# Kernel tuning notes

Measured on AMD Instinct MI355X. Metric: run time of the kernel, lower is better.

## Reference

```python
import jax, jax.numpy as jnp
import numpy as np
from jax import lax

D = 384      # embd_d
L = 4        # num_blocks
B = 64
SHW, THW = 24, 12
NS, NT = SHW * SHW, THW * THW   # 576, 144
EPS = 1e-5


def _ln(x, g, b):
    mu = jnp.mean(x, axis=-1, keepdims=True)
    var = jnp.mean(jnp.square(x - mu), axis=-1, keepdims=True)
    return (x - mu) * lax.rsqrt(var + EPS) * g + b


def setup_inputs() -> dict:
    key = jax.random.key(0)
    ks = iter(jax.random.split(key, 64))
    f32 = jnp.float32
    def nrm(shape, s=0.02):
        return jax.random.normal(next(ks), shape, dtype=f32) * s
    inp = {
        'search': jax.random.normal(next(ks), (B, NS, D), dtype=f32),
        'target': jax.random.normal(next(ks), (B, NT, D), dtype=f32),
        # learned tokens / positional params
        'cls': nrm((1, 1, D), 1.0),
        'search_pos': nrm((1, NS, D), 0.5),
        'target_pos': nrm((1, NT, D), 0.5),
        # stacked per-block params [L, ...]
        'ln1_g': jnp.ones((L, D), f32), 'ln1_b': jnp.zeros((L, D), f32),
        'Wq': nrm((L, D, D)), 'bq': jnp.zeros((L, D), f32),
        'Wk': nrm((L, D, D)), 'bk': jnp.zeros((L, D), f32),
        'Wv': nrm((L, D, D)), 'bv': jnp.zeros((L, D), f32),
        'ln2_g': jnp.ones((L, D), f32), 'ln2_b': jnp.zeros((L, D), f32),
        'W1': nrm((L, D, 2 * D)), 'b1': jnp.zeros((L, 2 * D), f32),
        'W2': nrm((L, 2 * D, D)), 'b2': jnp.zeros((L, D), f32),
        # head
        'lnf_g': jnp.ones((D,), f32), 'lnf_b': jnp.zeros((D,), f32),
        'Wl1': nrm((D, D)), 'bl1': jnp.zeros((D,), f32),
        'Wl2': nrm((D, 1)), 'bl2': jnp.zeros((1,), f32),
    }
    return inp


def reference(search, target, cls, search_pos, target_pos,
              ln1_g, ln1_b, Wq, bq, Wk, bk, Wv, bv,
              ln2_g, ln2_b, W1, b1, W2, b2,
              lnf_g, lnf_b, Wl1, bl1, Wl2, bl2):
    scale = D ** (-0.5)  # note: full embed dim, as in source
    x = jnp.concatenate([
        jnp.broadcast_to(cls, (B, 1, D)),
        search + search_pos,
        target + target_pos,
    ], axis=1)  # [B, 1+Ns+Nt, D]

    def block(x, p):
        l1g, l1b, wq, bq_, wk, bk_, wv, bv_, l2g, l2b, w1, b1_, w2, b2_ = p
        y = _ln(x, l1g, l1b)
        q = y @ wq + bq_
        k = y @ wk + bk_
        v = y @ wv + bv_
        attn = jax.nn.softmax(jnp.einsum('bid,bjd->bij', q, k) * scale, axis=-1)
        x = x + jnp.einsum('bij,bjd->bid', attn, v)
        h = _ln(x, l2g, l2b)
        x = x + (jax.nn.gelu(h @ w1 + b1_, approximate=False) @ w2 + b2_)
        return x, None

    x, _ = lax.scan(block, x, (ln1_g, ln1_b, Wq, bq, Wk, bk, Wv, bv,
                               ln2_g, ln2_b, W1, b1, W2, b2))
    h = _ln(x[:, 0], lnf_g, lnf_b)          # cls token [B, D]
    h = jax.nn.relu(h @ Wl1 + bl1)
    return h @ Wl2 + bl2                     # [B, 1]
```

## Files before the change

### kernel.cpp

```cpp
#include <hip/hip_runtime.h>
#include <hip/hip_bf16.h>
#include <math.h>

#define DD 384
#define NBATCH 64
#define NSEQ 721
#define NROWS (NBATCH*NSEQ)
#define NLAYER 4
#define VTW 736

typedef __bf16 bf16_t;
typedef __bf16 bf16x8 __attribute__((ext_vector_type(8)));
typedef float  f32x4  __attribute__((ext_vector_type(4)));

static __device__ __forceinline__ void split_bf16(float v, bf16_t& h, bf16_t& l) {
    h = (bf16_t)v;
    l = (bf16_t)(v - (float)h);
}
static __device__ __forceinline__ bf16x8 bzero8() {
    bf16x8 v = {(bf16_t)0.f,(bf16_t)0.f,(bf16_t)0.f,(bf16_t)0.f,
                (bf16_t)0.f,(bf16_t)0.f,(bf16_t)0.f,(bf16_t)0.f};
    return v;
}
static __device__ __forceinline__ void gload16(const void* g, void* l) {
    __builtin_amdgcn_global_load_lds(
        (const __attribute__((address_space(1))) unsigned int*)g,
        (__attribute__((address_space(3))) unsigned int*)l, 16, 0, 0);
}
static __device__ __forceinline__ int xcd_swz(int nwg) {
    int orig = blockIdx.x;
    int q = nwg >> 3, r = nwg & 7;
    int xcd = orig & 7, within = orig >> 3;
    int base = (xcd < r) ? xcd*(q+1) : r*(q+1) + (xcd - r)*q;
    return base + within;
}
static __device__ __forceinline__ void ln_from_partials(const float* ss, const float* ss2,
                                                        int row, float& mu, float& rstd) {
    float s = 0.f, q2 = 0.f;
    #pragma unroll
    for (int k = 0; k < 6; ++k) { s += ss[k*NROWS + row]; q2 += ss2[k*NROWS + row]; }
    mu = s * (1.f/DD);
    float var = q2 * (1.f/DD) - mu*mu;
    rstd = rsqrtf(var + 1e-5f);
}

__global__ __launch_bounds__(256) void build_x_kernel(const float* __restrict__ search,
                               const float* __restrict__ target,
                               const float* __restrict__ cls,
                               const float* __restrict__ spos,
                               const float* __restrict__ tpos,
                               bf16_t* __restrict__ xh, bf16_t* __restrict__ xl,
                               float* __restrict__ wss, float* __restrict__ wss2) {
    int wave = threadIdx.x >> 6, lane = threadIdx.x & 63;
    int row = blockIdx.x * 4 + wave;
    if (row >= NROWS) return;
    int b = row / NSEQ, n = row % NSEQ;
    float s = 0.f, q2 = 0.f;
    #pragma unroll
    for (int i = 0; i < 6; ++i) {
        int d = lane + 64*i;
        float val;
        if (n == 0)        val = cls[d];
        else if (n <= 576) val = search[((size_t)b*576 + (n-1))*DD + d] + spos[(size_t)(n-1)*DD + d];
        else               val = target[((size_t)b*144 + (n-577))*DD + d] + tpos[(size_t)(n-577)*DD + d];
        bf16_t h, l;
        split_bf16(val, h, l);
        xh[(size_t)row*DD + d] = h;
        xl[(size_t)row*DD + d] = l;
        s += val; q2 += val*val;
    }
    #pragma unroll
    for (int m = 1; m < 64; m <<= 1) { s += __shfl_xor(s, m); q2 += __shfl_xor(q2, m); }
    if (lane == 0) {
        wss[row] = s; wss2[row] = q2;
        #pragma unroll
        for (int k = 1; k < 6; ++k) { wss[k*NROWS + row] = 0.f; wss2[k*NROWS + row] = 0.f; }
    }
}

__global__ void transpose_split_kernel(const float* __restrict__ src,
                                       const float* __restrict__ g,
                                       bf16_t* __restrict__ dh,
                                       bf16_t* __restrict__ dl,
                                       int K, int N) {
    int idx = blockIdx.x * blockDim.x + threadIdx.x;
    if (idx >= K*N) return;
    int k = idx / N, n = idx % N;
    float v = src[idx];
    if (g) v *= g[k];
    bf16_t h, l;
    split_bf16(v, h, l);
    dh[(size_t)n*K + k] = h;
    dl[(size_t)n*K + k] = l;
}

__global__ void colsum_kernel(const float* __restrict__ W, const float* __restrict__ g,
                              const float* __restrict__ b, const float* __restrict__ bias,
                              float* __restrict__ c1, float* __restrict__ c2,
                              int K, int N, int outStride, int outOff) {
    int l = blockIdx.y;
    int n = blockIdx.x * 256 + threadIdx.x;
    if (n >= N) return;
    const float* Wl = W + (size_t)l*K*N;
    const float* gl = g + (size_t)l*K;
    const float* bl = b + (size_t)l*K;
    float s1 = 0.f, s2 = 0.f;
    for (int k = 0; k < K; ++k) {
        float w = Wl[(size_t)k*N + n];
        s1 = fmaf(gl[k], w, s1);
        s2 = fmaf(bl[k], w, s2);
    }
    c1[(size_t)l*outStride + outOff + n] = s1;
    c2[(size_t)l*outStride + outOff + n] = s2 + bias[(size_t)l*N + n];
}

static __device__ __forceinline__ void gemm_core(
        const bf16_t* __restrict__ ah, const bf16_t* __restrict__ al,
        const bf16_t* __restrict__ bh, const bf16_t* __restrict__ bl,
        bf16_t (&ls)[2][32][64][8],
        int m0, int n0, int K, f32x4 (&acc)[4][4]) {
    int t = threadIdx.x;
    int w = t >> 6, lane = t & 63;
    int c = lane & 15, g = lane >> 4;
    int wr = w >> 1, wc = w & 1;
    const bf16_t* src0 = (w==0) ? ah : (w==1) ? al : (w==2) ? bh : bl;
    int base_rc = (w < 2) ? m0 : n0;
    const bf16_t* srcbase = src0 + (size_t)(base_rc + c)*K + 8*g;

    int ksteps = K >> 5;
    #pragma unroll
    for (int i = 0; i < 8; ++i)
        gload16(srcbase + (size_t)(16*i)*K, &ls[0][w*8 + i][0][0]);

    for (int kt = 0; kt < ksteps; ++kt) {
        int cur = kt & 1;
        if (kt + 1 < ksteps) {
            int k0n = (kt + 1) << 5;
            #pragma unroll
            for (int i = 0; i < 8; ++i)
                gload16(srcbase + (size_t)(16*i)*K + k0n, &ls[cur^1][w*8 + i][0][0]);
            asm volatile("s_waitcnt vmcnt(8)" ::: "memory");
        } else {
            asm volatile("s_waitcnt vmcnt(0)" ::: "memory");
        }
        __builtin_amdgcn_sched_barrier(0);
        __builtin_amdgcn_s_barrier();
        __builtin_amdgcn_sched_barrier(0);
        bf16x8 af_h[4], af_l[4], bf_h[4], bf_l[4];
        #pragma unroll
        for (int i = 0; i < 4; ++i) {
            af_h[i] = *(const bf16x8*)&ls[cur][     4*wr + i][lane][0];
            af_l[i] = *(const bf16x8*)&ls[cur][ 8 + 4*wr + i][lane][0];
            bf_h[i] = *(const bf16x8*)&ls[cur][16 + 4*wc + i][lane][0];
            bf_l[i] = *(const bf16x8*)&ls[cur][24 + 4*wc + i][lane][0];
        }
        #pragma unroll
        for (int i = 0; i < 4; ++i)
            #pragma unroll
            for (int j = 0; j < 4; ++j) {
                acc[i][j] = __builtin_amdgcn_mfma_f32_16x16x32_bf16(af_h[i], bf_h[j], acc[i][j], 0,0,0);
                acc[i][j] = __builtin_amdgcn_mfma_f32_16x16x32_bf16(af_h[i], bf_l[j], acc[i][j], 0,0,0);
                acc[i][j] = __builtin_amdgcn_mfma_f32_16x16x32_bf16(af_l[i], bf_h[j], acc[i][j], 0,0,0);
            }
        __builtin_amdgcn_sched_barrier(0);
        __builtin_amdgcn_s_barrier();
    }
}

__global__ __launch_bounds__(256, 2) void gemm_qkv(
        const bf16_t* __restrict__ ah, const bf16_t* __restrict__ al,
        const bf16_t* __restrict__ bh, const bf16_t* __restrict__ bl,
        const float* __restrict__ ss, const float* __restrict__ ss2,
        const float* __restrict__ c1, const float* __restrict__ c2,
        bf16_t* __restrict__ qout, bf16_t* __restrict__ kout,
        bf16_t* __restrict__ vth, bf16_t* __restrict__ vtl,
        int M, int nwg) {
    __shared__ __align__(16) bf16_t ls[2][32][64][8];
    int wgid = xcd_swz(nwg);
    int m0 = (wgid / 9) * 128, n0 = (wgid % 9) * 128;
    f32x4 zero4 = {0.f,0.f,0.f,0.f};
    f32x4 acc[4][4];
    #pragma unroll
    for (int i = 0; i < 4; ++i)
        #pragma unroll
        for (int j = 0; j < 4; ++j) acc[i][j] = zero4;
    gemm_core(ah, al, bh, bl, ls, m0, n0, DD, acc);

    int t = threadIdx.x, w = t >> 6, lane = t & 63;
    int c = lane & 15, g = lane >> 4;
    int wr = w >> 1, wc = w & 1;
    float rmu[16], rrs[16];
    #pragma unroll
    for (int i = 0; i < 4; ++i)
        #pragma unroll
        for (int r = 0; r < 4; ++r) {
            int row = m0 + 64*wr + 16*i + 4*g + r;
            float mu = 0.f, rstd = 1.f;
            if (row < M) ln_from_partials(ss, ss2, row, mu, rstd);
            rmu[i*4+r] = mu; rrs[i*4+r] = rstd;
        }
    int seg = n0 / 384;
    int segoff = seg * 384;
    #pragma unroll
    for (int j = 0; j < 4; ++j) {
        int nglob = n0 + 64*wc + 16*j + c;
        int nloc = nglob - segoff;
        float C1 = c1[nglob], C2 = c2[nglob];
        #pragma unroll
        for (int i = 0; i < 4; ++i) {
            int rbase = m0 + 64*wr + 16*i + 4*g;
            #pragma unroll
            for (int r = 0; r < 4; ++r) {
                int row = rbase + r;
                if (row >= M) continue;
                float val = rrs[i*4+r]*(acc[i][j][r] - rmu[i*4+r]*C1) + C2;
                if (seg == 0) {
                    qout[(size_t)row*DD + nloc] = (bf16_t)val;
                } else if (seg == 1) {
                    kout[(size_t)row*DD + nloc] = (bf16_t)val;
                } else {
                    int bl_ = row / NSEQ;
                    int tok = row - bl_*NSEQ;
                    bf16_t h, l;
                    split_bf16(val, h, l);
                    size_t o = ((size_t)(bl_*DD + nloc))*VTW + tok;
                    vth[o] = h;
                    vtl[o] = l;
                }
            }
        }
    }
}

template<int EPI, int NT>
__global__ __launch_bounds__(256, 2) void gemm_mfma(
        const bf16_t* __restrict__ ah, const bf16_t* __restrict__ al,
        const bf16_t* __restrict__ bh, const bf16_t* __restrict__ bl,
        const float* __restrict__ ss, const float* __restrict__ ss2,
        const float* __restrict__ c1, const float* __restrict__ c2,
        const float* __restrict__ bias,
        const bf16_t* __restrict__ resh, const bf16_t* __restrict__ resl,
        bf16_t* __restrict__ o1, bf16_t* __restrict__ o2,
        float* __restrict__ wss, float* __restrict__ wss2,
        int M, int N, int K, int nwg) {
    __shared__ __align__(16) bf16_t ls[2][32][64][8];
    int wgid = xcd_swz(nwg);
    int m0 = (wgid / NT) * 128, n0 = (wgid % NT) * 128;
    f32x4 zero4 = {0.f,0.f,0.f,0.f};
    f32x4 acc[4][4];
    #pragma unroll
    for (int i = 0; i < 4; ++i)
        #pragma unroll
        for (int j = 0; j < 4; ++j) acc[i][j] = zero4;
    gemm_core(ah, al, bh, bl, ls, m0, n0, K, acc);

    int t = threadIdx.x, w = t >> 6, lane = t & 63;
    int c = lane & 15, g = lane >> 4;
    int wr = w >> 1, wc = w & 1;

    if (EPI == 2) {
        float rmu[16], rrs[16];
        #pragma unroll
        for (int i = 0; i < 4; ++i)
            #pragma unroll
            for (int r = 0; r < 4; ++r) {
                int row = m0 + 64*wr + 16*i + 4*g + r;
                float mu = 0.f, rstd = 1.f;
                if (row < M) ln_from_partials(ss, ss2, row, mu, rstd);
                rmu[i*4+r] = mu; rrs[i*4+r] = rstd;
            }
        #pragma unroll
        for (int j = 0; j < 4; ++j) {
            int n = n0 + 64*wc + 16*j + c;
            float C1 = c1[n], C2 = c2[n];
            #pragma unroll
            for (int i = 0; i < 4; ++i) {
                int rbase = m0 + 64*wr + 16*i + 4*g;
                #pragma unroll
                for (int r = 0; r < 4; ++r) {
                    int row = rbase + r;
                    if (row >= M) continue;
                    float val = rrs[i*4+r]*(acc[i][j][r] - rmu[i*4+r]*C1) + C2;
                    val = 0.5f*val*(1.0f + erff(val*0.70710678118654752f));
                    bf16_t h, l;
                    split_bf16(val, h, l);
                    size_t o = (size_t)row*N + n;
                    o1[o] = h;
                    o2[o] = l;
                }
            }
        }
    } else {
        int slot = (wgid % NT) + 3*wc;
        #pragma unroll
        for (int i = 0; i < 4; ++i)
            #pragma unroll
            for (int r = 0; r < 4; ++r) {
                int row = m0 + 64*wr + 16*i + 4*g + r;
                if (row >= M) continue;
                float s = 0.f, q2 = 0.f;
                #pragma unroll
                for (int j = 0; j < 4; ++j) {
                    int n = n0 + 64*wc + 16*j + c;
                    size_t o = (size_t)row*N + n;
                    float val = acc[i][j][r] + bias[n] + (float)resh[o] + (float)resl[o];
                    bf16_t h, l;
                    split_bf16(val, h, l);
                    o1[o] = h;
                    o2[o] = l;
                    s += val; q2 += val*val;
                }
                #pragma unroll
                for (int m = 1; m < 16; m <<= 1) { s += __shfl_xor(s, m); q2 += __shfl_xor(q2, m); }
                if (c == 0) {
                    wss[slot*NROWS + row] = s;
                    wss2[slot*NROWS + row] = q2;
                }
            }
    }
}

__global__ __launch_bounds__(256, 2) void attn_mfma(
        const bf16_t* __restrict__ qh, const bf16_t* __restrict__ kh,
        const bf16_t* __restrict__ vth, const bf16_t* __restrict__ vtl,
        bf16_t* __restrict__ xh, bf16_t* __restrict__ xl,
        float* __restrict__ wss, float* __restrict__ wss2, int nwg) {
    __shared__ __align__(16) char smem[73728];
    bf16_t* kf = (bf16_t*)smem;
    char* vhp = smem + 24576;
    char* vlp = smem + 49152;

    int t = threadIdx.x, w = t >> 6, lane = t & 63;
    int c = lane & 15, g = lane >> 4;
    int wgid = xcd_swz(nwg);
    int bl_ = wgid / 12;
    int q0 = (wgid % 12) * 64;
    size_t bb = (size_t)bl_ * NSEQ;
    int qrow = q0 + 16*w + c;
    bool qok = (qrow < NSEQ);
    const float scale = 0.05103103630798287f;
    int vswz = (c ^ (c >> 2)) & 3;
    int dma_dd  = lane >> 2;
    int dma_kv8 = (lane & 3) ^ ((dma_dd ^ (dma_dd >> 2)) & 3);

    bf16x8 qf[12];
    #pragma unroll
    for (int ks = 0; ks < 12; ++ks) {
        if (qok) qf[ks] = *(const bf16x8*)(qh + (bb + qrow)*DD + 32*ks + 8*g);
        else     qf[ks] = bzero8();
    }

    f32x4 zero4 = {0.f,0.f,0.f,0.f};
    f32x4 oacc[24];
    #pragma unroll
    for (int i = 0; i < 24; ++i) oacc[i] = zero4;
    float m_run = -1e30f, l_run = 0.f;

    #pragma unroll
    for (int i = 0; i < 6; ++i) {
        int s = i*4 + w;
        int ks = s >> 1, mf = s & 1;
        gload16(kh + (bb + (size_t)(16*mf + c))*DD + 32*ks + 8*g, kf + s*512);
    }

    for (int kt = 0; kt < 23; ++kt) {
        int kv0 = kt * 32;
        asm volatile("s_waitcnt vmcnt(0)" ::: "memory");
        __builtin_amdgcn_s_barrier();
        #pragma unroll
        for (int i = 0; i < 6; ++i) {
            int s = i*4 + w;
            size_t gro = ((size_t)(bl_*DD + 16*s + dma_dd))*VTW + kv0 + 8*dma_kv8;
            gload16(vth + gro, (bf16_t*)vhp + s*512);
            gload16(vtl + gro, (bf16_t*)vlp + s*512);
        }
        f32x4 sacc[2];
        sacc[0] = zero4; sacc[1] = zero4;
        #pragma unroll
        for (int ks = 0; ks < 12; ++ks) {
            bf16x8 a0 = *(const bf16x8*)(kf + ((size_t)(2*ks+0)*64 + lane)*8);
            bf16x8 a1 = *(const bf16x8*)(kf + ((size_t)(2*ks+1)*64 + lane)*8);
            sacc[0] = __builtin_amdgcn_mfma_f32_16x16x32_bf16(a0, qf[ks], sacc[0], 0,0,0);
            sacc[1] = __builtin_amdgcn_mfma_f32_16x16x32_bf16(a1, qf[ks], sacc[1], 0,0,0);
        }
        float p[2][4];
        float mx = -1e30f;
        #pragma unroll
        for (int mf = 0; mf < 2; ++mf)
            #pragma unroll
            for (int r = 0; r < 4; ++r) {
                float sv = sacc[mf][r] * scale;
                int kv = kv0 + 16*mf + 4*g + r;
                if (kv >= NSEQ) sv = -1e30f;
                p[mf][r] = sv;
                mx = fmaxf(mx, sv);
            }
        mx = fmaxf(mx, __shfl_xor(mx, 16));
        mx = fmaxf(mx, __shfl_xor(mx, 32));
        float m_new = fmaxf(m_run, mx);
        float corr = __expf(m_run - m_new);
        float psum = 0.f;
        #pragma unroll
        for (int mf = 0; mf < 2; ++mf)
            #pragma unroll
            for (int r = 0; r < 4; ++r) {
                float pv = __expf(p[mf][r] - m_new);
                p[mf][r] = pv;
                psum += pv;
            }
        psum += __shfl_xor(psum, 16);
        psum += __shfl_xor(psum, 32);
        l_run = l_run * corr + psum;
        m_run = m_new;
        #pragma unroll
        for (int i = 0; i < 24; ++i) oacc[i] *= corr;
        bf16x8 ph, pl;
        #pragma unroll
        for (int mf = 0; mf < 2; ++mf)
            #pragma unroll
            for (int r = 0; r < 4; ++r) {
                bf16_t hh, ll;
                split_bf16(p[mf][r], hh, ll);
                ph[mf*4 + r] = hh;
                pl[mf*4 + r] = ll;
            }
        asm volatile("s_waitcnt vmcnt(0)" ::: "memory");
        __builtin_amdgcn_s_barrier();
        if (kt + 1 < 23) {
            int kv0n = kv0 + 32;
            #pragma unroll
            for (int i = 0; i < 6; ++i) {
                int s = i*4 + w;
                int ks = s >> 1, mf = s & 1;
                gload16(kh + (bb + (size_t)(kv0n + 16*mf + c))*DD + 32*ks + 8*g, kf + s*512);
            }
        }
        #pragma unroll
        for (int mf = 0; mf < 24; ++mf) {
            int dr = 16*mf + c;
            const char* vb  = vhp + dr*64;
            const char* vb2 = vlp + dr*64;
            int o0 = ((((g>>1)     ^ vswz) << 4) | (8*(g&1)));
            int o1 = (((2 + (g>>1)) ^ vswz) << 4) | (8*(g&1));
            union { uint2 u[2]; bf16x8 v; } va, vc2;
            va.u[0]  = *(const uint2*)(vb  + o0);
            va.u[1]  = *(const uint2*)(vb  + o1);
            vc2.u[0] = *(const uint2*)(vb2 + o0);
            vc2.u[1] = *(const uint2*)(vb2 + o1);
            oacc[mf] = __builtin_amdgcn_mfma_f32_16x16x32_bf16(va.v,  ph, oacc[mf], 0,0,0);
            oacc[mf] = __builtin_amdgcn_mfma_f32_16x16x32_bf16(va.v,  pl, oacc[mf], 0,0,0);
            oacc[mf] = __builtin_amdgcn_mfma_f32_16x16x32_bf16(vc2.v, ph, oacc[mf], 0,0,0);
        }
    }
    float inv = 1.f / l_run;
    float s = 0.f, q2 = 0.f;
    if (qok) {
        bf16_t* xhr = xh + (bb + qrow)*DD;
        bf16_t* xlr = xl + (bb + qrow)*DD;
        #pragma unroll
        for (int mf = 0; mf < 24; ++mf)
            #pragma unroll
            for (int r = 0; r < 4; ++r) {
                int d = 16*mf + 4*g + r;
                float xv = (float)xhr[d] + (float)xlr[d] + oacc[mf][r]*inv;
                bf16_t h, l;
                split_bf16(xv, h, l);
                xhr[d] = h;
                xlr[d] = l;
                s += xv; q2 += xv*xv;
            }
    }
    s += __shfl_xor(s, 16);  q2 += __shfl_xor(q2, 16);
    s += __shfl_xor(s, 32);  q2 += __shfl_xor(q2, 32);
    if (qok && g == 0) {
        int rowL = bl_*NSEQ + qrow;
        wss[rowL] = s; wss2[rowL] = q2;
        #pragma unroll
        for (int k = 1; k < 6; ++k) { wss[k*NROWS + rowL] = 0.f; wss2[k*NROWS + rowL] = 0.f; }
    }
}

__global__ __launch_bounds__(384) void head_kernel(const bf16_t* __restrict__ xh,
    const bf16_t* __restrict__ xl,
    const float* __restrict__ g, const float* __restrict__ bb,
    const float* __restrict__ Wl1, const float* __restrict__ bl1,
    const float* __restrict__ Wl2, const float* __restrict__ bl2,
    float* __restrict__ outp) {
    __shared__ float yv[384];
    __shared__ float r1[6], r2[6], r3[6];
    int b = blockIdx.x, t = threadIdx.x;
    size_t o = (size_t)b*NSEQ*DD + t;
    float v = (float)xh[o] + (float)xl[o];
    float s = v;
    #pragma unroll
    for (int m = 1; m < 64; m <<= 1) s += __shfl_xor(s, m);
    if ((t & 63) == 0) r1[t>>6] = s;
    __syncthreads();
    float mu = (r1[0]+r1[1]+r1[2]+r1[3]+r1[4]+r1[5]) * (1.f/384.f);
    float dd = v - mu;
    float sq = dd*dd;
    #pragma unroll
    for (int m = 1; m < 64; m <<= 1) sq += __shfl_xor(sq, m);
    if ((t & 63) == 0) r2[t>>6] = sq;
    __syncthreads();
    float var = (r2[0]+r2[1]+r2[2]+r2[3]+r2[4]+r2[5]) * (1.f/384.f);
    float rstd = rsqrtf(var + 1e-5f);
    yv[t] = dd*rstd*g[t] + bb[t];
    __syncthreads();
    float acc = bl1[t];
    for (int d2 = 0; d2 < 384; d2++) acc = fmaf(yv[d2], Wl1[d2*384 + t], acc);
    acc = fmaxf(acc, 0.f);
    float oo = acc * Wl2[t];
    #pragma unroll
    for (int m = 1; m < 64; m <<= 1) oo += __shfl_xor(oo, m);
    if ((t & 63) == 0) r3[t>>6] = oo;
    __syncthreads();
    if (t == 0) outp[b] = r3[0]+r3[1]+r3[2]+r3[3]+r3[4]+r3[5] + bl2[0];
}

extern "C" void kernel_launch(void* const* d_in, const int* in_sizes, int n_in,
                              void* d_out, int out_size, void* d_ws, size_t ws_size,
                              hipStream_t stream) {
    const float* search = (const float*)d_in[0];
    const float* target = (const float*)d_in[1];
    const float* cls    = (const float*)d_in[2];
    const float* spos   = (const float*)d_in[3];
    const float* tpos   = (const float*)d_in[4];
    const float* ln1_g  = (const float*)d_in[5];
    const float* ln1_b  = (const float*)d_in[6];
    const float* Wq     = (const float*)d_in[7];
    const float* bq     = (const float*)d_in[8];
    const float* Wk     = (const float*)d_in[9];
    const float* bk     = (const float*)d_in[10];
    const float* Wv     = (const float*)d_in[11];
    const float* bv     = (const float*)d_in[12];
    const float* ln2_g  = (const float*)d_in[13];
    const float* ln2_b  = (const float*)d_in[14];
    const float* W1     = (const float*)d_in[15];
    const float* b1     = (const float*)d_in[16];
    const float* W2     = (const float*)d_in[17];
    const float* b2     = (const float*)d_in[18];
    const float* lnf_g  = (const float*)d_in[19];
    const float* lnf_b  = (const float*)d_in[20];
    const float* Wl1    = (const float*)d_in[21];
    const float* bl1    = (const float*)d_in[22];
    const float* Wl2    = (const float*)d_in[23];
    const float* bl2    = (const float*)d_in[24];

    size_t off = 0;
    char* base = (char*)d_ws;
    auto alloc = [&](size_t bytes) -> void* {
        void* p = base + off;
        off += (bytes + 255) & ~(size_t)255;
        return p;
    };

    bf16_t* xh = (bf16_t*)alloc((size_t)NROWS * DD * 2);
    bf16_t* xl = (bf16_t*)alloc((size_t)NROWS * DD * 2);
    float* ssum  = (float*)alloc((size_t)6*NROWS*4);
    float* ssum2 = (float*)alloc((size_t)6*NROWS*4);

    const int SQKV = 1152*DD;
    const int SM = DD*768;
    bf16_t* wqkvh = (bf16_t*)alloc((size_t)4*SQKV*2);
    bf16_t* wqkvl = (bf16_t*)alloc((size_t)4*SQKV*2);
    bf16_t* w1h = (bf16_t*)alloc((size_t)4*SM*2);
    bf16_t* w1l = (bf16_t*)alloc((size_t)4*SM*2);
    bf16_t* w2h = (bf16_t*)alloc((size_t)4*SM*2);
    bf16_t* w2l = (bf16_t*)alloc((size_t)4*SM*2);
    float* cqkv1 = (float*)alloc((size_t)4*1152*4);
    float* cqkv2 = (float*)alloc((size_t)4*1152*4);
    float* cm11  = (float*)alloc((size_t)4*768*4);
    float* cm12  = (float*)alloc((size_t)4*768*4);

    const size_t qB  = (size_t)NSEQ*DD*2;
    const size_t vB  = (size_t)DD*VTW*2;
    const size_t mB  = (size_t)NSEQ*768*2;
    const size_t perB = 2*qB + 2*vB;
    size_t avail = (ws_size > off + 262144) ? (ws_size - off - 262144) : 0;
    int G = (int)(avail / perB);
    if (G > NBATCH) G = NBATCH;
    if (G < 1) G = 1;

    char* U = (char*)alloc(perB * G);
    bf16_t* qhB  = (bf16_t*)U;
    bf16_t* khB  = (bf16_t*)(U + qB*G);
    bf16_t* vth  = (bf16_t*)(U + 2*qB*G);
    bf16_t* vtl  = (bf16_t*)(U + 2*qB*G + vB*G);
    bf16_t* midh = (bf16_t*)U;
    bf16_t* midl = (bf16_t*)(U + mB*G);

    build_x_kernel<<<(NROWS+3)/4, 256, 0, stream>>>(search, target, cls, spos, tpos,
                                                    xh, xl, ssum, ssum2);

    const int SQ = DD*DD;
    for (int l = 0; l < NLAYER; ++l) {
        bf16_t* dsth = wqkvh + (size_t)l*SQKV;
        bf16_t* dstl = wqkvl + (size_t)l*SQKV;
        transpose_split_kernel<<<(SQ+255)/256, 256, 0, stream>>>(Wq + (size_t)l*SQ, ln1_g + l*DD, dsth,          dstl,          DD, DD);
        transpose_split_kernel<<<(SQ+255)/256, 256, 0, stream>>>(Wk + (size_t)l*SQ, ln1_g + l*DD, dsth + 384*DD, dstl + 384*DD, DD, DD);
        transpose_split_kernel<<<(SQ+255)/256, 256, 0, stream>>>(Wv + (size_t)l*SQ, ln1_g + l*DD, dsth + 768*DD, dstl + 768*DD, DD, DD);
        transpose_split_kernel<<<(SM+255)/256, 256, 0, stream>>>(W1 + (size_t)l*SM, ln2_g + l*DD, w1h + (size_t)l*SM, w1l + (size_t)l*SM, DD, 768);
        transpose_split_kernel<<<(SM+255)/256, 256, 0, stream>>>(W2 + (size_t)l*SM, nullptr,      w2h + (size_t)l*SM, w2l + (size_t)l*SM, 768, DD);
    }
    colsum_kernel<<<dim3(2, NLAYER), 256, 0, stream>>>(Wq, ln1_g, ln1_b, bq, cqkv1, cqkv2, DD, DD, 1152, 0);
    colsum_kernel<<<dim3(2, NLAYER), 256, 0, stream>>>(Wk, ln1_g, ln1_b, bk, cqkv1, cqkv2, DD, DD, 1152, 384);
    colsum_kernel<<<dim3(2, NLAYER), 256, 0, stream>>>(Wv, ln1_g, ln1_b, bv, cqkv1, cqkv2, DD, DD, 1152, 768);
    colsum_kernel<<<dim3(3, NLAYER), 256, 0, stream>>>(W1, ln2_g, ln2_b, b1, cm11, cm12, DD, 768, 768, 0);

    for (int l = 0; l < NLAYER; ++l) {
        for (int b0 = 0; b0 < NBATCH; b0 += G) {
            int cb = (NBATCH - b0 < G) ? (NBATCH - b0) : G;
            int Mc = cb * NSEQ;
            bf16_t* xch = xh + (size_t)b0 * NSEQ * DD;
            bf16_t* xcl = xl + (size_t)b0 * NSEQ * DD;
            float* ssc  = ssum  + (size_t)b0 * NSEQ;
            float* ssc2 = ssum2 + (size_t)b0 * NSEQ;
            int mtiles = (Mc + 127)/128;
            int nwgQKV = 9*mtiles, nwgM1 = 6*mtiles, nwgM2 = 3*mtiles, nwgA = 12*cb;

            gemm_qkv<<<nwgQKV, 256, 0, stream>>>(xch, xcl,
                    wqkvh + (size_t)l*SQKV, wqkvl + (size_t)l*SQKV,
                    ssc, ssc2, cqkv1 + l*1152, cqkv2 + l*1152,
                    qhB, khB, vth, vtl, Mc, nwgQKV);
            attn_mfma<<<nwgA, 256, 0, stream>>>(qhB, khB, vth, vtl, xch, xcl,
                    ssc, ssc2, nwgA);
            gemm_mfma<2,6><<<nwgM1, 256, 0, stream>>>(xch, xcl,
                    w1h + (size_t)l*SM, w1l + (size_t)l*SM,
                    ssc, ssc2, cm11 + l*768, cm12 + l*768, nullptr,
                    nullptr, nullptr, midh, midl, nullptr, nullptr, Mc, 768, DD, nwgM1);
            gemm_mfma<3,3><<<nwgM2, 256, 0, stream>>>(midh, midl,
                    w2h + (size_t)l*SM, w2l + (size_t)l*SM,
                    nullptr, nullptr, nullptr, nullptr, b2 + l*DD,
                    xch, xcl, xch, xcl, ssc, ssc2, Mc, DD, 768, nwgM2);
        }
    }
    head_kernel<<<NBATCH, 384, 0, stream>>>(xh, xl, lnf_g, lnf_b, Wl1, bl1, Wl2, bl2, (float*)d_out);
}
```

Baseline: 3.860 ms.

## Store transposed V contiguously with LDS-staged writes; single-buffer GEMM LDS for occupancy

The transposed V buffer moves from a per-batch padded layout to one contiguous [D, MP] layout across the chunk. Full tiles now stage the hi/lo split through swizzled LDS so they can issue 16-byte coalesced stores instead of scattered 2-byte writes; the attention kernel's V loads are re-indexed to match. Separately, the GEMM core drops LDS double buffering in favour of a single buffer with two syncthreads per k-step, and launch bounds rise to 4 waves per SIMD to gain occupancy. The cost is that global loads no longer overlap with MFMA work inside a workgroup, and register limits get tighter.

```diff
diff --git a/kernel.cpp b/kernel.cpp
--- a/kernel.cpp
+++ b/kernel.cpp
@@ -7,7 +7,6 @@
 #define NSEQ 721
 #define NROWS (NBATCH*NSEQ)
 #define NLAYER 4
-#define VTW 736
 
 typedef __bf16 bf16_t;
 typedef __bf16 bf16x8 __attribute__((ext_vector_type(8)));
@@ -117,7 +116,7 @@
 static __device__ __forceinline__ void gemm_core(
         const bf16_t* __restrict__ ah, const bf16_t* __restrict__ al,
         const bf16_t* __restrict__ bh, const bf16_t* __restrict__ bl,
-        bf16_t (&ls)[2][32][64][8],
+        bf16_t (&ls)[32][64][8],
         int m0, int n0, int K, f32x4 (&acc)[4][4]) {
     int t = threadIdx.x;
     int w = t >> 6, lane = t & 63;
@@ -128,31 +127,20 @@
     const bf16_t* srcbase = src0 + (size_t)(base_rc + c)*K + 8*g;
 
     int ksteps = K >> 5;
-    #pragma unroll
-    for (int i = 0; i < 8; ++i)
-        gload16(srcbase + (size_t)(16*i)*K, &ls[0][w*8 + i][0][0]);
-
     for (int kt = 0; kt < ksteps; ++kt) {
-        int cur = kt & 1;
-        if (kt + 1 < ksteps) {
-            int k0n = (kt + 1) << 5;
-            #pragma unroll
-            for (int i = 0; i < 8; ++i)
-                gload16(srcbase + (size_t)(16*i)*K + k0n, &ls[cur^1][w*8 + i][0][0]);
-            asm volatile("s_waitcnt vmcnt(8)" ::: "memory");
-        } else {
-            asm volatile("s_waitcnt vmcnt(0)" ::: "memory");
-        }
-        __builtin_amdgcn_sched_barrier(0);
-        __builtin_amdgcn_s_barrier();
-        __builtin_amdgcn_sched_barrier(0);
+        int k0 = kt << 5;
+        __syncthreads();
+        #pragma unroll
+        for (int i = 0; i < 8; ++i)
+            gload16(srcbase + (size_t)(16*i)*K + k0, &ls[w*8 + i][0][0]);
+        __syncthreads();
         bf16x8 af_h[4], af_l[4], bf_h[4], bf_l[4];
         #pragma unroll
         for (int i = 0; i < 4; ++i) {
-            af_h[i] = *(const bf16x8*)&ls[cur][     4*wr + i][lane][0];
-            af_l[i] = *(const bf16x8*)&ls[cur][ 8 + 4*wr + i][lane][0];
-            bf_h[i] = *(const bf16x8*)&ls[cur][16 + 4*wc + i][lane][0];
-            bf_l[i] = *(const bf16x8*)&ls[cur][24 + 4*wc + i][lane][0];
+            af_h[i] = *(const bf16x8*)&ls[     4*wr + i][lane][0];
+            af_l[i] = *(const bf16x8*)&ls[ 8 + 4*wr + i][lane][0];
+            bf_h[i] = *(const bf16x8*)&ls[16 + 4*wc + i][lane][0];
+            bf_l[i] = *(const bf16x8*)&ls[24 + 4*wc + i][lane][0];
         }
         #pragma unroll
         for (int i = 0; i < 4; ++i)
@@ -162,20 +150,18 @@
                 acc[i][j] = __builtin_amdgcn_mfma_f32_16x16x32_bf16(af_h[i], bf_l[j], acc[i][j], 0,0,0);
                 acc[i][j] = __builtin_amdgcn_mfma_f32_16x16x32_bf16(af_l[i], bf_h[j], acc[i][j], 0,0,0);
             }
-        __builtin_amdgcn_sched_barrier(0);
-        __builtin_amdgcn_s_barrier();
-    }
-}
-
-__global__ __launch_bounds__(256, 2) void gemm_qkv(
+    }
+}
+
+__global__ __launch_bounds__(256, 4) void gemm_qkv(
         const bf16_t* __restrict__ ah, const bf16_t* __restrict__ al,
         const bf16_t* __restrict__ bh, const bf16_t* __restrict__ bl,
         const float* __restrict__ ss, const float* __restrict__ ss2,
         const float* __restrict__ c1, const float* __restrict__ c2,
         bf16_t* __restrict__ qout, bf16_t* __restrict__ kout,
         bf16_t* __restrict__ vth, bf16_t* __restrict__ vtl,
-        int M, int nwg) {
-    __shared__ __align__(16) bf16_t ls[2][32][64][8];
+        int M, int MP, int nwg) {
+    __shared__ __align__(16) bf16_t ls[32][64][8];
     int wgid = xcd_swz(nwg);
     int m0 = (wgid / 9) * 128, n0 = (wgid % 9) * 128;
     f32x4 zero4 = {0.f,0.f,0.f,0.f};
@@ -200,40 +186,90 @@
             rmu[i*4+r] = mu; rrs[i*4+r] = rstd;
         }
     int seg = n0 / 384;
-    int segoff = seg * 384;
-    #pragma unroll
-    for (int j = 0; j < 4; ++j) {
-        int nglob = n0 + 64*wc + 16*j + c;
-        int nloc = nglob - segoff;
-        float C1 = c1[nglob], C2 = c2[nglob];
-        #pragma unroll
-        for (int i = 0; i < 4; ++i) {
-            int rbase = m0 + 64*wr + 16*i + 4*g;
-            #pragma unroll
-            for (int r = 0; r < 4; ++r) {
-                int row = rbase + r;
-                if (row >= M) continue;
-                float val = rrs[i*4+r]*(acc[i][j][r] - rmu[i*4+r]*C1) + C2;
-                if (seg == 0) {
-                    qout[(size_t)row*DD + nloc] = (bf16_t)val;
-                } else if (seg == 1) {
-                    kout[(size_t)row*DD + nloc] = (bf16_t)val;
-                } else {
-                    int bl_ = row / NSEQ;
-                    int tok = row - bl_*NSEQ;
-                    bf16_t h, l;
-                    split_bf16(val, h, l);
-                    size_t o = ((size_t)(bl_*DD + nloc))*VTW + tok;
-                    vth[o] = h;
-                    vtl[o] = l;
+    if (seg < 2) {
+        bf16_t* outb = (seg == 0) ? qout : kout;
+        int segoff = seg * 384;
+        #pragma unroll
+        for (int j = 0; j < 4; ++j) {
+            int nglob = n0 + 64*wc + 16*j + c;
+            int nloc = nglob - segoff;
+            float C1 = c1[nglob], C2 = c2[nglob];
+            #pragma unroll
+            for (int i = 0; i < 4; ++i) {
+                int rbase = m0 + 64*wr + 16*i + 4*g;
+                #pragma unroll
+                for (int r = 0; r < 4; ++r) {
+                    int row = rbase + r;
+                    if (row >= M) continue;
+                    float val = rrs[i*4+r]*(acc[i][j][r] - rmu[i*4+r]*C1) + C2;
+                    outb[(size_t)row*DD + nloc] = (bf16_t)val;
                 }
             }
         }
+    } else {
+        int vbase = n0 - 768;
+        bool tail = (m0 + 128 > M);
+        if (!tail) {
+            bf16_t* LST = &ls[0][0][0];
+            #pragma unroll
+            for (int pass = 0; pass < 2; ++pass) {
+                __syncthreads();
+                #pragma unroll
+                for (int j = 0; j < 4; ++j) {
+                    int d = 64*wc + 16*j + c;
+                    int nglob = 768 + vbase + 0; (void)nglob;
+                    float C1 = c1[n0 + 64*wc + 16*j + c];
+                    float C2 = c2[n0 + 64*wc + 16*j + c];
+                    #pragma unroll
+                    for (int i = 0; i < 4; ++i)
+                        #pragma unroll
+                        for (int r = 0; r < 4; ++r) {
+                            int tok = 64*wr + 16*i + 4*g + r;
+                            float val = rrs[i*4+r]*(acc[i][j][r] - rmu[i*4+r]*C1) + C2;
+                            bf16_t h, l;
+                            split_bf16(val, h, l);
+                            LST[d*128 + (tok ^ ((d & 15) << 3))] = pass ? l : h;
+                        }
+                }
+                __syncthreads();
+                bf16_t* outp = pass ? vtl : vth;
+                #pragma unroll
+                for (int p = 0; p < 8; ++p) {
+                    int chunk = t + 256*p;
+                    int d = chunk >> 4;
+                    int tok0 = (chunk & 15) * 8;
+                    uint4 v = *(const uint4*)&LST[d*128 + (tok0 ^ ((d & 15) << 3))];
+                    *(uint4*)(outp + (size_t)(vbase + d)*MP + m0 + tok0) = v;
+                }
+            }
+        } else {
+            #pragma unroll
+            for (int j = 0; j < 4; ++j) {
+                int d = vbase + 64*wc + 16*j + c;
+                float C1 = c1[n0 + 64*wc + 16*j + c];
+                float C2 = c2[n0 + 64*wc + 16*j + c];
+                #pragma unroll
+                for (int i = 0; i < 4; ++i) {
+                    int rbase = m0 + 64*wr + 16*i + 4*g;
+                    #pragma unroll
+                    for (int r = 0; r < 4; ++r) {
+                        int row = rbase + r;
+                        if (row >= M) continue;
+                        float val = rrs[i*4+r]*(acc[i][j][r] - rmu[i*4+r]*C1) + C2;
+                        bf16_t h, l;
+                        split_bf16(val, h, l);
+                        size_t o = (size_t)d*MP + row;
+                        vth[o] = h;
+                        vtl[o] = l;
+                    }
+                }
+            }
+        }
     }
 }
 
 template<int EPI, int NT>
-__global__ __launch_bounds__(256, 2) void gemm_mfma(
+__global__ __launch_bounds__(256, 4) void gemm_mfma(
         const bf16_t* __restrict__ ah, const bf16_t* __restrict__ al,
         const bf16_t* __restrict__ bh, const bf16_t* __restrict__ bl,
         const float* __restrict__ ss, const float* __restrict__ ss2,
@@ -243,7 +279,7 @@
         bf16_t* __restrict__ o1, bf16_t* __restrict__ o2,
         float* __restrict__ wss, float* __restrict__ wss2,
         int M, int N, int K, int nwg) {
-    __shared__ __align__(16) bf16_t ls[2][32][64][8];
+    __shared__ __align__(16) bf16_t ls[32][64][8];
     int wgid = xcd_swz(nwg);
     int m0 = (wgid / NT) * 128, n0 = (wgid % NT) * 128;
     f32x4 zero4 = {0.f,0.f,0.f,0.f};
@@ -324,7 +360,7 @@
         const bf16_t* __restrict__ qh, const bf16_t* __restrict__ kh,
         const bf16_t* __restrict__ vth, const bf16_t* __restrict__ vtl,
         bf16_t* __restrict__ xh, bf16_t* __restrict__ xl,
-        float* __restrict__ wss, float* __restrict__ wss2, int nwg) {
+        float* __restrict__ wss, float* __restrict__ wss2, int MP, int nwg) {
     __shared__ __align__(16) char smem[73728];
     bf16_t* kf = (bf16_t*)smem;
     char* vhp = smem + 24576;
@@ -370,7 +406,7 @@
         #pragma unroll
         for (int i = 0; i < 6; ++i) {
             int s = i*4 + w;
-            size_t gro = ((size_t)(bl_*DD + 16*s + dma_dd))*VTW + kv0 + 8*dma_kv8;
+            size_t gro = (size_t)(16*s + dma_dd)*MP + bb + kv0 + 8*dma_kv8;
             gload16(vth + gro, (bf16_t*)vhp + s*512);
             gload16(vtl + gro, (bf16_t*)vlp + s*512);
         }
@@ -574,19 +610,24 @@
     float* cm12  = (float*)alloc((size_t)4*768*4);
 
     const size_t qB  = (size_t)NSEQ*DD*2;
-    const size_t vB  = (size_t)DD*VTW*2;
     const size_t mB  = (size_t)NSEQ*768*2;
-    const size_t perB = 2*qB + 2*vB;
+    const size_t perB = 2*qB + 4*(size_t)DD*NSEQ + 4096;
     size_t avail = (ws_size > off + 262144) ? (ws_size - off - 262144) : 0;
     int G = (int)(avail / perB);
     if (G > NBATCH) G = NBATCH;
     if (G < 1) G = 1;
 
-    char* U = (char*)alloc(perB * G);
+    int MPi = (int)((((size_t)G*NSEQ + 7) & ~(size_t)7) + 32);
+    size_t vBytes = (size_t)DD * MPi * 2;
+    size_t sizeQKV = 2*qB*(size_t)G + 2*vBytes;
+    size_t sizeMid = 2*mB*(size_t)G;
+    size_t Usz = (sizeQKV > sizeMid ? sizeQKV : sizeMid);
+
+    char* U = (char*)alloc(Usz);
     bf16_t* qhB  = (bf16_t*)U;
     bf16_t* khB  = (bf16_t*)(U + qB*G);
     bf16_t* vth  = (bf16_t*)(U + 2*qB*G);
-    bf16_t* vtl  = (bf16_t*)(U + 2*qB*G + vB*G);
+    bf16_t* vtl  = (bf16_t*)(U + 2*qB*G + vBytes);
     bf16_t* midh = (bf16_t*)U;
     bf16_t* midl = (bf16_t*)(U + mB*G);
 
@@ -622,9 +663,9 @@
             gemm_qkv<<<nwgQKV, 256, 0, stream>>>(xch, xcl,
                     wqkvh + (size_t)l*SQKV, wqkvl + (size_t)l*SQKV,
                     ssc, ssc2, cqkv1 + l*1152, cqkv2 + l*1152,
-                    qhB, khB, vth, vtl, Mc, nwgQKV);
+                    qhB, khB, vth, vtl, Mc, MPi, nwgQKV);
             attn_mfma<<<nwgA, 256, 0, stream>>>(qhB, khB, vth, vtl, xch, xcl,
-                    ssc, ssc2, nwgA);
+                    ssc, ssc2, MPi, nwgA);
             gemm_mfma<2,6><<<nwgM1, 256, 0, stream>>>(xch, xcl,
                     w1h + (size_t)l*SM, w1l + (size_t)l*SM,
                     ssc, ssc2, cm11 + l*768, cm12 + l*768, nullptr,
```

New measurement: 4.044 ms. +4.8%, slower.
